# Optimization experiments

Measured on AMD Instinct MI355X. Metric: run time of the kernel, lower is better.

Reference implementation:

```python
import jax, jax.numpy as jnp
import numpy as np

ALPHA = 0.2  # tf.nn.leaky_relu default

def leaky(x):
    return jnp.where(x >= 0, x, ALPHA * x)

def segment_softmax(score, seg, num_segments):
    m = jax.ops.segment_max(score, seg, num_segments=num_segments)
    e = jnp.exp(score - m[seg])
    denom = jax.ops.segment_sum(e, seg, num_segments=num_segments)
    return e / denom[seg]

def setup_inputs() -> dict:
    key = jax.random.key(0)
    ks = jax.random.split(key, 8)
    E, NE, NR, D, U = 500000, 100000, 1000, 128, 128
    return {
        "h_index": jax.random.randint(ks[0], (E,), 0, NE),
        "r_index": jax.random.randint(ks[1], (E,), 0, NR),
        "t_index": jax.random.randint(ks[2], (E,), 0, NE),
        "entity_embeddings": jax.random.normal(ks[3], (NE, D), jnp.float32),
        "relation_embeddings": jax.random.normal(ks[4], (NR, D), jnp.float32),
        "W": jax.random.normal(ks[5], (3 * D, U), jnp.float32) * 0.05,
        "a": jax.random.normal(ks[6], (U, 1), jnp.float32) * 0.1,
        "a_b": jnp.zeros((1,), jnp.float32),
        "bias": jnp.zeros((U,), jnp.float32),
    }

def reference(h_index, r_index, t_index, entity_embeddings, relation_embeddings, W, a, a_b, bias):
    num_entities = entity_embeddings.shape[0]
    h = entity_embeddings[h_index]          # [E, D]
    r = relation_embeddings[r_index]        # [E, D]
    t = entity_embeddings[t_index]          # [E, D]
    feats = jnp.concatenate([h, r, t], axis=-1) @ W  # [E, U]
    # att_kernel Dense(1, activation=leaky_relu), then wrapped again in att_activation
    score = leaky(leaky(feats @ a + a_b))[:, 0]      # [E]
    alpha = segment_softmax(score, h_index, num_entities)
    msg = feats * alpha[:, None]                     # gcn_mapper: edge features * weight
    reduced = jax.ops.segment_sum(msg, h_index, num_segments=num_entities)  # [NE, U]
    out = reduced + bias                             # identity_updater returns reduced_msg
    return jax.nn.relu(out)
```

## Files before the change

### kernel.cpp

```cpp
#include <hip/hip_runtime.h>
#include <hip/hip_bf16.h>

#define ALPHA2 0.04f

typedef __attribute__((ext_vector_type(8))) short short8;
typedef __attribute__((ext_vector_type(4))) float floatx4;
typedef __attribute__((ext_vector_type(8))) unsigned short ushort8;

__device__ __forceinline__ unsigned short f2bf(float f) {
    unsigned u = __float_as_uint(f);
    unsigned r = (u + 0x7fffu + ((u >> 16) & 1u)) >> 16;
    return (unsigned short)r;
}
__device__ __forceinline__ float bf2f(unsigned short h) {
    return __uint_as_float((unsigned)h << 16);
}

__device__ __forceinline__ void async_copy16(const float* g, float* lds_base) {
    __builtin_amdgcn_global_load_lds(
        (const __attribute__((address_space(1))) unsigned int*)g,
        (__attribute__((address_space(3))) unsigned int*)lds_base, 16, 0, 0);
}


__global__ void k_prep(const float* __restrict__ W, unsigned short* __restrict__ Bfr,
                       int* __restrict__ count, int NE,
                       unsigned long long* __restrict__ tstate, int NBt) {
    int idx = blockIdx.x * blockDim.x + threadIdx.x;
    if (idx < 3 * 128 * 128) {
        int kk = idx & 7, n = (idx >> 3) & 127, g = idx >> 10;
        int slice = g >> 4, kc = (g >> 2) & 3, quad = g & 3;
        int k = kc * 32 + quad * 8 + kk;
        Bfr[idx] = f2bf(W[(size_t)(slice * 128 + k) * 128 + n]);
    }
    if (idx < NE) count[idx] = 0;
    if (idx < NBt) tstate[idx] = 0ull;
}

__global__ __launch_bounds__(256, 4) void k_gemm_all(
        const float* __restrict__ ent, const float* __restrict__ rel,
        const unsigned short* __restrict__ Bfr,
        unsigned short* __restrict__ Pb, unsigned short* __restrict__ Qb,
        unsigned short* __restrict__ Rb,
        float* __restrict__ s1, float* __restrict__ s3, float* __restrict__ s2,
        const float* __restrict__ avec, int NE, int NR, int NBcnt, int NBent,
        int total,
        const int* __restrict__ hidx, int* __restrict__ count,
        int* __restrict__ rank, int E) {
    __shared__ __align__(16) float Ash[64 * 128];
    int tid = threadIdx.x;
    int b = blockIdx.x;

    int cb_before = (int)(((long long)b * NBcnt) / total);
    int cb_after = (int)(((long long)(b + 1) * NBcnt) / total);
    if (cb_after > cb_before) {
        int base_e = cb_before * 1024;
        #pragma unroll
        for (int k2 = 0; k2 < 4; ++k2) {
            int e = base_e + k2 * 256 + tid;
            if (e < E) rank[e] = atomicAdd(count + hidx[e], 1);
        }
        return;
    }
    int gb = b - cb_after;

    bool isEnt = gb < NBent;
    const float* In = isEnt ? ent : rel;
    int nrows = isEnt ? NE : NR;
    int rowbase = (isEnt ? gb : gb - NBent) * 64;

    int wave = tid >> 6, lane = tid & 63;

    #pragma unroll
    for (int i = 0; i < 8; ++i) {
        int r = wave * 16 + i * 2 + (lane >> 5);
        int grow = rowbase + r;
        if (grow > nrows - 1) grow = nrows - 1;
        int c = (lane & 31) ^ (r & 7);
        async_copy16(In + (size_t)grow * 128 + c * 4,
                     Ash + (size_t)(wave * 16 + i * 2) * 128);
    }
    __syncthreads();

    int m16 = lane & 15, quad = lane >> 4;
    int rs = wave * 16;
    int R = rs + m16, sw = R & 7;
    const float4* rowp = (const float4*)(Ash + (size_t)R * 128);

    float av[8];
    #pragma unroll
    for (int j = 0; j < 8; ++j) av[j] = avec[j * 16 + m16];

    int nphase = isEnt ? 2 : 1;
    for (int ph = 0; ph < nphase; ++ph) {
        int slice; unsigned short* Out; float* svec;
        if (isEnt) { slice = ph ? 2 : 0; Out = ph ? Qb : Pb; svec = ph ? s3 : s1; }
        else       { slice = 1; Out = Rb; svec = s2; }

        floatx4 acc[8];
        #pragma unroll
        for (int j = 0; j < 8; ++j) acc[j] = (floatx4){0.f, 0.f, 0.f, 0.f};

        short8 bf0[8], bf1[8];
        auto loadB = [&](int kc, short8* dst) {
            const unsigned short* bb =
                Bfr + (size_t)((slice * 4 + kc) * 4 + quad) * 1024 + m16 * 8;
            #pragma unroll
            for (int j = 0; j < 8; ++j) dst[j] = *(const short8*)(bb + j * 128);
        };
        auto doMfma = [&](int kc, short8* bf) {
            int c0 = kc * 8 + quad * 2;
            float4 fa = rowp[c0 ^ sw];
            float4 fb = rowp[(c0 + 1) ^ sw];
            short8 af;
            af[0] = (short)f2bf(fa.x); af[1] = (short)f2bf(fa.y);
            af[2] = (short)f2bf(fa.z); af[3] = (short)f2bf(fa.w);
            af[4] = (short)f2bf(fb.x); af[5] = (short)f2bf(fb.y);
            af[6] = (short)f2bf(fb.z); af[7] = (short)f2bf(fb.w);
            #pragma unroll
            for (int j = 0; j < 8; ++j)
                acc[j] = __builtin_amdgcn_mfma_f32_16x16x32_bf16(af, bf[j], acc[j], 0, 0, 0);
        };
        loadB(0, bf0);
        loadB(1, bf1);
        doMfma(0, bf0);
        loadB(2, bf0);
        doMfma(1, bf1);
        loadB(3, bf1);
        doMfma(2, bf0);
        doMfma(3, bf1);

        #pragma unroll
        for (int reg = 0; reg < 4; ++reg) {
            int row = rowbase + rs + quad * 4 + reg;
            float part = 0.f;
            ushort8 v;
            #pragma unroll
            for (int j = 0; j < 8; ++j) {
                float x = acc[j][reg];
                part = fmaf(x, av[j], part);
                v[j] = f2bf(x);
            }
            #pragma unroll
            for (int off = 1; off < 16; off <<= 1) part += __shfl_xor(part, off);
            if (row < nrows) {
                *(ushort8*)(Out + (size_t)row * 128 + m16 * 8) = v;
                if (m16 == 0) svec[row] = part;
            }
        }
    }
}

__device__ __forceinline__ int block_incl_scan256(int s, int* sh, int t) {
    sh[t] = s; __syncthreads();
    #pragma unroll
    for (int off = 1; off < 256; off <<= 1) {
        int x = 0;
        if (t >= off) x = sh[t - off];
        __syncthreads();
        sh[t] += x;
        __syncthreads();
    }
    return sh[t];
}

__global__ __launch_bounds__(256) void k_scan1(const int* __restrict__ count, int NE,
                                               unsigned long long* __restrict__ tstate,
                                               int* __restrict__ rowstart, int E) {
    __shared__ int sh[256];
    int b = blockIdx.x, t = threadIdx.x;
    int base = b * 1024 + t * 4;
    int v[4]; int s = 0;
    #pragma unroll
    for (int j = 0; j < 4; ++j) { int i = base + j; v[j] = (i < NE) ? count[i] : 0; s += v[j]; }
    int incl = block_incl_scan256(s, sh, t);
    if (t == 0) {
        unsigned long long pk = (1ull << 32) | (unsigned)sh[255];
        __hip_atomic_store(&tstate[b], pk, __ATOMIC_RELEASE, __HIP_MEMORY_SCOPE_AGENT);
    }
    int myval = 0;
    if (t < b) {
        unsigned long long pk;
        for (;;) {
            pk = __hip_atomic_load(&tstate[t], __ATOMIC_ACQUIRE, __HIP_MEMORY_SCOPE_AGENT);
            if (pk >> 32) break;
            __builtin_amdgcn_s_sleep(1);
        }
        myval = (int)(unsigned)pk;
    }
    __syncthreads();
    sh[t] = myval; __syncthreads();
    for (int off = 128; off > 0; off >>= 1) {
        if (t < off) sh[t] += sh[t + off];
        __syncthreads();
    }
    int excl = sh[0] + incl - s;
    #pragma unroll
    for (int j = 0; j < 4; ++j) {
        int i = base + j;
        if (i < NE) { rowstart[i] = excl; excl += v[j]; }
    }
    if (b == 0 && t == 0) rowstart[NE] = E;
}

__global__ void k_scatter_rt(const int* __restrict__ h, const int* __restrict__ r,
                             const int* __restrict__ t,
                             const int* __restrict__ rowstart,
                             const int* __restrict__ rank,
                             unsigned* __restrict__ rt, int E) {
    int e = blockIdx.x * blockDim.x + threadIdx.x;
    if (e >= E) return;
    rt[rowstart[h[e]] + rank[e]] = ((unsigned)r[e] << 17) | (unsigned)t[e];
}

__global__ __launch_bounds__(256) void k_aggregate(const int* __restrict__ rowstart,
                                                   const unsigned* __restrict__ rt,
                                                   const unsigned short* __restrict__ Pb,
                                                   const unsigned short* __restrict__ Qb,
                                                   const unsigned short* __restrict__ Rb,
                                                   const float* __restrict__ s1,
                                                   const float* __restrict__ s2,
                                                   const float* __restrict__ s3,
                                                   const float* __restrict__ a_b,
                                                   const float* __restrict__ bias,
                                                   float* __restrict__ out, int NE) {
    int gid = blockIdx.x * blockDim.x + threadIdx.x;
    int n = gid >> 4;
    int sl = gid & 15;
    if (n >= NE) return;
    int start = rowstart[n], end = rowstart[n + 1];
    int c0 = sl * 8;
    float base = s1[n] + a_b[0];
    float acc[8] = {};
    float evsum = 0.f;
    int i = start;
    for (; i + 4 <= end; i += 4) {
        unsigned u0 = rt[i], u1 = rt[i + 1], u2 = rt[i + 2], u3 = rt[i + 3];
        unsigned t0 = u0 & 0x1FFFFu, r0i = u0 >> 17;
        unsigned t1 = u1 & 0x1FFFFu, r1i = u1 >> 17;
        unsigned t2 = u2 & 0x1FFFFu, r2i = u2 >> 17;
        unsigned t3 = u3 & 0x1FFFFu, r3i = u3 >> 17;
        ushort8 q0 = *(const ushort8*)(Qb + (size_t)t0 * 128 + c0);
        ushort8 rr0 = *(const ushort8*)(Rb + (size_t)r0i * 128 + c0);
        ushort8 q1 = *(const ushort8*)(Qb + (size_t)t1 * 128 + c0);
        ushort8 rr1 = *(const ushort8*)(Rb + (size_t)r1i * 128 + c0);
        ushort8 q2 = *(const ushort8*)(Qb + (size_t)t2 * 128 + c0);
        ushort8 rr2 = *(const ushort8*)(Rb + (size_t)r2i * 128 + c0);
        ushort8 q3 = *(const ushort8*)(Qb + (size_t)t3 * 128 + c0);
        ushort8 rr3 = *(const ushort8*)(Rb + (size_t)r3i * 128 + c0);
        float x0 = base + s2[r0i] + s3[t0];
        float x1 = base + s2[r1i] + s3[t1];
        float x2 = base + s2[r2i] + s3[t2];
        float x3 = base + s2[r3i] + s3[t3];
        x0 = (x0 >= 0.f) ? x0 : ALPHA2 * x0;
        x1 = (x1 >= 0.f) ? x1 : ALPHA2 * x1;
        x2 = (x2 >= 0.f) ? x2 : ALPHA2 * x2;
        x3 = (x3 >= 0.f) ? x3 : ALPHA2 * x3;
        float ev0 = __expf(x0), ev1 = __expf(x1);
        float ev2 = __expf(x2), ev3 = __expf(x3);
        evsum += (ev0 + ev1) + (ev2 + ev3);
        #pragma unroll
        for (int j = 0; j < 8; ++j) {
            acc[j] = fmaf(ev0, bf2f(q0[j]) + bf2f(rr0[j]), acc[j]);
            acc[j] = fmaf(ev1, bf2f(q1[j]) + bf2f(rr1[j]), acc[j]);
            acc[j] = fmaf(ev2, bf2f(q2[j]) + bf2f(rr2[j]), acc[j]);
            acc[j] = fmaf(ev3, bf2f(q3[j]) + bf2f(rr3[j]), acc[j]);
        }
    }
    for (; i < end; ++i) {
        unsigned u0 = rt[i];
        unsigned t0 = u0 & 0x1FFFFu, r0i = u0 >> 17;
        ushort8 q0 = *(const ushort8*)(Qb + (size_t)t0 * 128 + c0);
        ushort8 rr0 = *(const ushort8*)(Rb + (size_t)r0i * 128 + c0);
        float x0 = base + s2[r0i] + s3[t0];
        x0 = (x0 >= 0.f) ? x0 : ALPHA2 * x0;
        float ev0 = __expf(x0);
        evsum += ev0;
        #pragma unroll
        for (int j = 0; j < 8; ++j)
            acc[j] = fmaf(ev0, bf2f(q0[j]) + bf2f(rr0[j]), acc[j]);
    }
    float bi[8];
    #pragma unroll
    for (int j = 0; j < 8; ++j) bi[j] = bias[j * 16 + sl];
    float o[8];
    if (end > start) {
        float inv = 1.f / evsum;
        ushort8 pb = *(const ushort8*)(Pb + (size_t)n * 128 + c0);
        #pragma unroll
        for (int j = 0; j < 8; ++j) o[j] = bf2f(pb[j]) + acc[j] * inv + bi[j];
    } else {
        #pragma unroll
        for (int j = 0; j < 8; ++j) o[j] = bi[j];
    }
    #pragma unroll
    for (int j = 0; j < 8; ++j)
        out[(size_t)n * 128 + j * 16 + sl] = fmaxf(o[j], 0.f);
}

static inline size_t align_up(size_t x, size_t a) { return (x + a - 1) / a * a; }

extern "C" void kernel_launch(void* const* d_in, const int* in_sizes, int n_in,
                              void* d_out, int out_size, void* d_ws, size_t ws_size,
                              hipStream_t stream) {
    const int* h_index = (const int*)d_in[0];
    const int* r_index = (const int*)d_in[1];
    const int* t_index = (const int*)d_in[2];
    const float* ent = (const float*)d_in[3];
    const float* rel = (const float*)d_in[4];
    const float* W = (const float*)d_in[5];
    const float* a = (const float*)d_in[6];
    const float* a_b = (const float*)d_in[7];
    const float* bias = (const float*)d_in[8];
    float* out = (float*)d_out;

    int E = in_sizes[0];
    int NE = in_sizes[3] / 128;
    int NR = in_sizes[4] / 128;

    char* p = (char*)d_ws;
    auto alloc = [&](size_t bytes) { char* q = p; p += align_up(bytes, 256); return (void*)q; };
    unsigned short* Pb = (unsigned short*)alloc((size_t)NE * 128 * 2);
    unsigned short* Qb = (unsigned short*)alloc((size_t)NE * 128 * 2);
    unsigned short* Rb = (unsigned short*)alloc((size_t)NR * 128 * 2);
    unsigned short* Bfr = (unsigned short*)alloc((size_t)3 * 128 * 128 * 2);
    float* s1 = (float*)alloc((size_t)NE * 4);
    float* s3 = (float*)alloc((size_t)NE * 4);
    float* s2 = (float*)alloc((size_t)NR * 4);
    int* count = (int*)alloc((size_t)NE * 4);
    int* rowstart = (int*)alloc((size_t)(NE + 1) * 4);
    int* rank = (int*)alloc((size_t)E * 4);
    int NB = (NE + 1023) / 1024;
    unsigned long long* tstate = (unsigned long long*)alloc((size_t)NB * 8);
    unsigned* rt = (unsigned*)alloc((size_t)E * 4);
    (void)ws_size; (void)n_in; (void)out_size;

    int nprep = (NE > 3 * 128 * 128) ? NE : 3 * 128 * 128;
    k_prep<<<(nprep + 255) / 256, 256, 0, stream>>>(W, Bfr, count, NE, tstate, NB);
    int NBent = (NE + 63) / 64, NBrel = (NR + 63) / 64;
    int NBgemm = NBent + NBrel;
    int NBcnt = (E + 1023) / 1024;
    int total = NBcnt + NBgemm;
    k_gemm_all<<<total, 256, 0, stream>>>(
        ent, rel, Bfr, Pb, Qb, Rb, s1, s3, s2, a, NE, NR, NBcnt, NBent, total,
        h_index, count, rank, E);
    k_scan1<<<NB, 256, 0, stream>>>(count, NE, tstate, rowstart, E);
    k_scatter_rt<<<(E + 255) / 256, 256, 0, stream>>>(h_index, r_index, t_index,
                                                      rowstart, rank, rt, E);
    k_aggregate<<<(NE * 16 + 255) / 256, 256, 0, stream>>>(rowstart, rt, Pb, Qb, Rb,
                                                           s1, s2, s3, a_b, bias,
                                                           out, NE);
}
```

Measured before the change: 190.5 us.

## Fuse scan and scatter kernels with per-tile ready flags; prefetch B before barrier

Merges the decoupled-lookback row-start scan and the edge scatter into one kernel. Scatter threads spin on a per-tile ready flag until the rowstart tile they need has been published, which removes one kernel launch and its inter-kernel gap. Separately, the GEMM kernel now issues its first two B-fragment loads before the LDS barrier so they overlap the async A copy. The spin-wait relies on forward progress of the lower-index scan blocks, which holds for this launch order but adds synchronization risk.

After: 360.4 us. 1.89x slower.

```diff
diff --git a/kernel.cpp b/kernel.cpp
--- a/kernel.cpp
+++ b/kernel.cpp
@@ -25,7 +25,8 @@
 
 __global__ void k_prep(const float* __restrict__ W, unsigned short* __restrict__ Bfr,
                        int* __restrict__ count, int NE,
-                       unsigned long long* __restrict__ tstate, int NBt) {
+                       unsigned long long* __restrict__ tstate,
+                       int* __restrict__ rdy, int NBt) {
     int idx = blockIdx.x * blockDim.x + threadIdx.x;
     if (idx < 3 * 128 * 128) {
         int kk = idx & 7, n = (idx >> 3) & 127, g = idx >> 10;
@@ -34,7 +35,7 @@
         Bfr[idx] = f2bf(W[(size_t)(slice * 128 + k) * 128 + n]);
     }
     if (idx < NE) count[idx] = 0;
-    if (idx < NBt) tstate[idx] = 0ull;
+    if (idx < NBt) { tstate[idx] = 0ull; rdy[idx] = 0; }
 }
 
 __global__ __launch_bounds__(256, 4) void k_gemm_all(
@@ -80,7 +81,6 @@
         async_copy16(In + (size_t)grow * 128 + c * 4,
                      Ash + (size_t)(wave * 16 + i * 2) * 128);
     }
-    __syncthreads();
 
     int m16 = lane & 15, quad = lane >> 4;
     int rs = wave * 16;
@@ -91,7 +91,20 @@
     #pragma unroll
     for (int j = 0; j < 8; ++j) av[j] = avec[j * 16 + m16];
 
+    short8 bf0[8], bf1[8];
+    auto loadB = [&](int slice, int kc, short8* dst) {
+        const unsigned short* bb =
+            Bfr + (size_t)((slice * 4 + kc) * 4 + quad) * 1024 + m16 * 8;
+        #pragma unroll
+        for (int j = 0; j < 8; ++j) dst[j] = *(const short8*)(bb + j * 128);
+    };
+
     int nphase = isEnt ? 2 : 1;
+    int slice0 = isEnt ? 0 : 1;
+    loadB(slice0, 0, bf0);
+    loadB(slice0, 1, bf1);
+    __syncthreads();
+
     for (int ph = 0; ph < nphase; ++ph) {
         int slice; unsigned short* Out; float* svec;
         if (isEnt) { slice = ph ? 2 : 0; Out = ph ? Qb : Pb; svec = ph ? s3 : s1; }
@@ -101,13 +114,6 @@
         #pragma unroll
         for (int j = 0; j < 8; ++j) acc[j] = (floatx4){0.f, 0.f, 0.f, 0.f};
 
-        short8 bf0[8], bf1[8];
-        auto loadB = [&](int kc, short8* dst) {
-            const unsigned short* bb =
-                Bfr + (size_t)((slice * 4 + kc) * 4 + quad) * 1024 + m16 * 8;
-            #pragma unroll
-            for (int j = 0; j < 8; ++j) dst[j] = *(const short8*)(bb + j * 128);
-        };
         auto doMfma = [&](int kc, short8* bf) {
             int c0 = kc * 8 + quad * 2;
             float4 fa = rowp[c0 ^ sw];
@@ -121,12 +127,14 @@
             for (int j = 0; j < 8; ++j)
                 acc[j] = __builtin_amdgcn_mfma_f32_16x16x32_bf16(af, bf[j], acc[j], 0, 0, 0);
         };
-        loadB(0, bf0);
-        loadB(1, bf1);
+        if (ph > 0) {
+            loadB(slice, 0, bf0);
+            loadB(slice, 1, bf1);
+        }
         doMfma(0, bf0);
-        loadB(2, bf0);
+        loadB(slice, 2, bf0);
         doMfma(1, bf1);
-        loadB(3, bf1);
+        loadB(slice, 3, bf1);
         doMfma(2, bf0);
         doMfma(3, bf1);
 
@@ -164,53 +172,68 @@
     return sh[t];
 }
 
-__global__ __launch_bounds__(256) void k_scan1(const int* __restrict__ count, int NE,
-                                               unsigned long long* __restrict__ tstate,
-                                               int* __restrict__ rowstart, int E) {
+__global__ __launch_bounds__(256) void k_scan_scatter(
+        const int* __restrict__ count, int NE, int NB,
+        unsigned long long* __restrict__ tstate, int* __restrict__ rdy,
+        int* __restrict__ rowstart, int E,
+        const int* __restrict__ h, const int* __restrict__ r,
+        const int* __restrict__ t, const int* __restrict__ rank,
+        unsigned* __restrict__ rt) {
     __shared__ int sh[256];
-    int b = blockIdx.x, t = threadIdx.x;
-    int base = b * 1024 + t * 4;
-    int v[4]; int s = 0;
-    #pragma unroll
-    for (int j = 0; j < 4; ++j) { int i = base + j; v[j] = (i < NE) ? count[i] : 0; s += v[j]; }
-    int incl = block_incl_scan256(s, sh, t);
-    if (t == 0) {
-        unsigned long long pk = (1ull << 32) | (unsigned)sh[255];
-        __hip_atomic_store(&tstate[b], pk, __ATOMIC_RELEASE, __HIP_MEMORY_SCOPE_AGENT);
-    }
-    int myval = 0;
-    if (t < b) {
-        unsigned long long pk;
-        for (;;) {
-            pk = __hip_atomic_load(&tstate[t], __ATOMIC_ACQUIRE, __HIP_MEMORY_SCOPE_AGENT);
-            if (pk >> 32) break;
-            __builtin_amdgcn_s_sleep(1);
-        }
-        myval = (int)(unsigned)pk;
-    }
-    __syncthreads();
-    sh[t] = myval; __syncthreads();
-    for (int off = 128; off > 0; off >>= 1) {
-        if (t < off) sh[t] += sh[t + off];
+    int b = blockIdx.x, tx = threadIdx.x;
+
+    if (b < NB) {
+        int base = b * 1024 + tx * 4;
+        int v[4]; int s = 0;
+        #pragma unroll
+        for (int j = 0; j < 4; ++j) { int i = base + j; v[j] = (i < NE) ? count[i] : 0; s += v[j]; }
+        int incl = block_incl_scan256(s, sh, tx);
+        if (tx == 0) {
+            unsigned long long pk = (1ull << 32) | (unsigned)sh[255];
+            __hip_atomic_store(&tstate[b], pk, __ATOMIC_RELEASE, __HIP_MEMORY_SCOPE_AGENT);
+        }
+        int myval = 0;
+        if (tx < b) {
+            unsigned long long pk;
+            for (;;) {
+                pk = __hip_atomic_load(&tstate[tx], __ATOMIC_ACQUIRE, __HIP_MEMORY_SCOPE_AGENT);
+                if (pk >> 32) break;
+                __builtin_amdgcn_s_sleep(1);
+            }
+            myval = (int)(unsigned)pk;
+        }
         __syncthreads();
-    }
-    int excl = sh[0] + incl - s;
-    #pragma unroll
-    for (int j = 0; j < 4; ++j) {
-        int i = base + j;
-        if (i < NE) { rowstart[i] = excl; excl += v[j]; }
-    }
-    if (b == 0 && t == 0) rowstart[NE] = E;
-}
-
-__global__ void k_scatter_rt(const int* __restrict__ h, const int* __restrict__ r,
-                             const int* __restrict__ t,
-                             const int* __restrict__ rowstart,
-                             const int* __restrict__ rank,
-                             unsigned* __restrict__ rt, int E) {
-    int e = blockIdx.x * blockDim.x + threadIdx.x;
-    if (e >= E) return;
-    rt[rowstart[h[e]] + rank[e]] = ((unsigned)r[e] << 17) | (unsigned)t[e];
+        sh[tx] = myval; __syncthreads();
+        for (int off = 128; off > 0; off >>= 1) {
+            if (tx < off) sh[tx] += sh[tx + off];
+            __syncthreads();
+        }
+        int excl = sh[0] + incl - s;
+        #pragma unroll
+        for (int j = 0; j < 4; ++j) {
+            int i = base + j;
+            if (i < NE) { rowstart[i] = excl; excl += v[j]; }
+        }
+        if (b == 0 && tx == 0) rowstart[NE] = E;
+        __syncthreads();
+        if (tx == 0)
+            __hip_atomic_store(&rdy[b], 1, __ATOMIC_RELEASE, __HIP_MEMORY_SCOPE_AGENT);
+    }
+
+    int base_e = b * 1024;
+    #pragma unroll
+    for (int k2 = 0; k2 < 4; ++k2) {
+        int e = base_e + k2 * 256 + tx;
+        if (e < E) {
+            int hi = h[e];
+            int tile = hi >> 10;
+            if (__hip_atomic_load(&rdy[tile], __ATOMIC_ACQUIRE, __HIP_MEMORY_SCOPE_AGENT) == 0) {
+                do { __builtin_amdgcn_s_sleep(2); }
+                while (__hip_atomic_load(&rdy[tile], __ATOMIC_ACQUIRE, __HIP_MEMORY_SCOPE_AGENT) == 0);
+            }
+            rt[rowstart[hi] + rank[e]] = ((unsigned)r[e] << 17) | (unsigned)t[e];
+        }
+    }
 }
 
 __global__ __launch_bounds__(256) void k_aggregate(const int* __restrict__ rowstart,
@@ -332,11 +355,12 @@
     int* rank = (int*)alloc((size_t)E * 4);
     int NB = (NE + 1023) / 1024;
     unsigned long long* tstate = (unsigned long long*)alloc((size_t)NB * 8);
+    int* rdy = (int*)alloc((size_t)NB * 4);
     unsigned* rt = (unsigned*)alloc((size_t)E * 4);
     (void)ws_size; (void)n_in; (void)out_size;
 
     int nprep = (NE > 3 * 128 * 128) ? NE : 3 * 128 * 128;
-    k_prep<<<(nprep + 255) / 256, 256, 0, stream>>>(W, Bfr, count, NE, tstate, NB);
+    k_prep<<<(nprep + 255) / 256, 256, 0, stream>>>(W, Bfr, count, NE, tstate, rdy, NB);
     int NBent = (NE + 63) / 64, NBrel = (NR + 63) / 64;
     int NBgemm = NBent + NBrel;
     int NBcnt = (E + 1023) / 1024;
@@ -344,9 +368,11 @@
     k_gemm_all<<<total, 256, 0, stream>>>(
         ent, rel, Bfr, Pb, Qb, Rb, s1, s3, s2, a, NE, NR, NBcnt, NBent, total,
         h_index, count, rank, E);
-    k_scan1<<<NB, 256, 0, stream>>>(count, NE, tstate, rowstart, E);
-    k_scatter_rt<<<(E + 255) / 256, 256, 0, stream>>>(h_index, r_index, t_index,
-                                                      rowstart, rank, rt, E);
+    int NBes = (E + 1023) / 1024;
+    int gridSS = (NBes > NB) ? NBes : NB;
+    k_scan_scatter<<<gridSS, 256, 0, stream>>>(count, NE, NB, tstate, rdy,
+                                               rowstart, E, h_index, r_index,
+                                               t_index, rank, rt);
     k_aggregate<<<(NE * 16 + 255) / 256, 256, 0, stream>>>(rowstart, rt, Pb, Qb, Rb,
                                                            s1, s2, s3, a_b, bias,
                                                            out, NE);
```
